# Kernel tuning notes

Hardware: AMD Instinct MI355X
Metric: run time of the kernel (lower is better)

## Reference

```python
import jax, jax.numpy as jnp
import numpy as np

DIM = 1024
HEADS = 16
DIM_HEAD = 64
SEQ = 2048
BATCH = 2
SCALE = DIM_HEAD ** -0.5
NEG = -jnp.finfo(jnp.float32).max


def setup_inputs() -> dict:
    key = jax.random.key(0)
    k1, k2, k3 = jax.random.split(key, 3)
    x = jax.random.normal(k1, (BATCH, SEQ, DIM), dtype=jnp.float32)
    w_qkv = jax.random.normal(k2, (DIM, 3 * HEADS * DIM_HEAD), dtype=jnp.float32) * 0.02
    w_out = jax.random.normal(k3, (HEADS * DIM_HEAD, DIM), dtype=jnp.float32) * 0.02
    b_out = jnp.zeros((DIM,), dtype=jnp.float32)
    return {"x": x, "w_qkv": w_qkv, "w_out": w_out, "b_out": b_out}


def reference(x, w_qkv, w_out, b_out):
    b, n, _ = x.shape
    qkv = x @ w_qkv  # [b, n, 3*h*d]
    q, k, v = jnp.split(qkv, 3, axis=-1)
    def to_heads(t):
        return t.reshape(b, n, HEADS, DIM_HEAD).transpose(0, 2, 1, 3)  # b h n d
    q, k, v = to_heads(q), to_heads(k), to_heads(v)
    q = q * SCALE
    dots = jnp.einsum('bhid,bhjd->bhij', q, k)  # materialized [b,h,n,n] scores
    causal_mask = jnp.triu(jnp.ones((n, n), dtype=bool), k=1)
    dots = jnp.where(causal_mask, NEG, dots)
    attn = jax.nn.softmax(dots, axis=-1)
    out = jnp.einsum('bhij,bhjd->bhid', attn, v)
    out = out.transpose(0, 2, 1, 3).reshape(b, n, HEADS * DIM_HEAD)
    return out @ w_out + b_out
```

## Files before the change

### kernel.cpp

```cpp
#include <hip/hip_runtime.h>
#include <cstdint>

typedef __attribute__((ext_vector_type(8))) short bfrag_t;
typedef __attribute__((ext_vector_type(4))) float f32x4_t;

#define MFMA16(a,b,c) __builtin_amdgcn_mfma_f32_16x16x32_bf16((a),(b),(c),0,0,0)

__device__ __forceinline__ unsigned short f2bf(float f){
  unsigned u = __float_as_uint(f);
  unsigned r = u + 0x7fffu + ((u >> 16) & 1u);
  return (unsigned short)(r >> 16);
}

__device__ __forceinline__ unsigned pk2bf(float a, float b){
  unsigned r;
  asm("v_cvt_pk_bf16_f32 %0, %1, %2" : "=v"(r) : "v"(a), "v"(b));
  return r;
}

__device__ __forceinline__ void gload16(const unsigned short* g, unsigned short* l){
  __builtin_amdgcn_global_load_lds(
      (const __attribute__((address_space(1))) unsigned int*)(const void*)g,
      (__attribute__((address_space(3))) unsigned int*)(void*)l,
      16, 0, 0);
}

__global__ __launch_bounds__(256) void k_prep(
    const float* __restrict__ x,     unsigned short* __restrict__ xbf,
    const float* __restrict__ wqkv,  unsigned short* __restrict__ wqkvT,
    const float* __restrict__ wout,  unsigned short* __restrict__ woutT)
{
  __shared__ unsigned short tile[32][33];
  const int bid = blockIdx.x;
  const int tid = threadIdx.x;

  if (bid < 2048){
    const int n4 = 4096*1024/4;
    int i = bid*256 + tid;
    #pragma unroll
    for(int it=0; it<2; it++, i += 2048*256){
      if (i < n4){
        float4 v = ((const float4*)x)[i];
        ushort4 o;
        o.x = f2bf(v.x); o.y = f2bf(v.y); o.z = f2bf(v.z); o.w = f2bf(v.w);
        ((ushort4*)xbf)[i] = o;
      }
    }
    return;
  }

  const float* in; unsigned short* out; int R, C, idx;
  if (bid < 5120){ in = wqkv; out = wqkvT; R = 1024; C = 3072; idx = bid - 2048; }
  else           { in = wout; out = woutT; R = 1024; C = 1024; idx = bid - 5120; }
  const int nbc = C >> 5;
  const int bc = (idx % nbc) * 32, br = (idx / nbc) * 32;
  const int tx = tid & 31, ty = tid >> 5;
  #pragma unroll
  for(int i=0;i<32;i+=8){
    tile[ty+i][tx] = f2bf(in[(size_t)(br+ty+i)*C + bc + tx]);
  }
  __syncthreads();
  #pragma unroll
  for(int i=0;i<32;i+=8){
    out[(size_t)(bc+ty+i)*R + br + tx] = tile[tx][ty+i];
  }
}

__global__ __launch_bounds__(256) void k_gemm1(
    const unsigned short* __restrict__ A,
    const unsigned short* __restrict__ Bt,
    unsigned short* __restrict__ Qo, unsigned short* __restrict__ Kimg,
    unsigned short* __restrict__ Vimg)
{
  __shared__ unsigned short ldsA[128*64];
  __shared__ unsigned short ldsB[128*64];

  const int tid = threadIdx.x;
  const int lane = tid & 63;
  const int w = tid >> 6;
  const int wr = w >> 1, wc = w & 1;
  const int col16 = lane & 15, g = lane >> 4;

  const int L = blockIdx.x;
  const int bm = (L / 24) * 128;
  const int bn = (L % 24) * 128;
  const int K = 1024;
  const int SWAP = (bn < 2048) ? 1 : 0;

  f32x4_t acc[4][4];
  #pragma unroll
  for(int i=0;i<4;i++)
    #pragma unroll
    for(int j=0;j<4;j++) acc[i][j] = (f32x4_t)0.0f;

  for(int k0=0; k0<K; k0+=64){
    __syncthreads();
    #pragma unroll
    for(int i=0; i<4; i++){
      int u = i*256 + tid;
      int row = u>>3, s = u&7, gs = s ^ (row&7);
      gload16(A + (size_t)(bm+row)*K + k0 + gs*8, ldsA + (i*256 + w*64)*8);
    }
    #pragma unroll
    for(int i=0; i<4; i++){
      int u = i*256 + tid;
      int row = u>>3, s = u&7, gs = s ^ (row&7);
      gload16(Bt + (size_t)(bn+row)*K + k0 + gs*8, ldsB + (i*256 + w*64)*8);
    }
    __syncthreads();
    #pragma unroll
    for(int kk=0; kk<2; kk++){
      bfrag_t af[4], bfr[4];
      #pragma unroll
      for(int mi=0;mi<4;mi++){
        int row = wr*64 + mi*16 + col16;
        int slot = (kk*4 + g) ^ (row&7);
        af[mi] = *(const bfrag_t*)(ldsA + row*64 + slot*8);
      }
      #pragma unroll
      for(int ni=0;ni<4;ni++){
        int row = wc*64 + ni*16 + col16;
        int slot = (kk*4 + g) ^ (row&7);
        bfr[ni] = *(const bfrag_t*)(ldsB + row*64 + slot*8);
      }
      if (SWAP){
        #pragma unroll
        for(int mi=0;mi<4;mi++)
          #pragma unroll
          for(int ni=0;ni<4;ni++)
            acc[mi][ni] = MFMA16(bfr[ni], af[mi], acc[mi][ni]);
      } else {
        #pragma unroll
        for(int mi=0;mi<4;mi++)
          #pragma unroll
          for(int ni=0;ni<4;ni++)
            acc[mi][ni] = MFMA16(af[mi], bfr[ni], acc[mi][ni]);
      }
    }
  }

  if (bn < 2048){
    const int which = bn >> 10;
    #pragma unroll
    for(int mi=0;mi<4;mi++){
      int s_full = bm + wr*64 + mi*16 + col16;
      int b = s_full >> 11, sq = s_full & 2047;
      #pragma unroll
      for(int ni=0;ni<4;ni++){
        int n0 = bn + wc*64 + ni*16 + g*4;
        int h = (n0 & 1023) >> 6;
        int d0 = n0 & 63;
        size_t bh = (size_t)(b*16 + h);
        float v0 = acc[mi][ni][0], v1 = acc[mi][ni][1];
        float v2 = acc[mi][ni][2], v3 = acc[mi][ni][3];
        if (which == 0){
          const float sc = 0.18033688f;
          uint2 pkd; pkd.x = pk2bf(v0*sc, v1*sc); pkd.y = pk2bf(v2*sc, v3*sc);
          *(uint2*)(Qo + (bh*2048 + sq)*64 + d0) = pkd;
        } else {
          int kt = sq >> 6, rr = sq & 63;
          int ks = rr >> 4, c16i = rr & 15;
          int dk = d0 >> 5, g3 = (d0 >> 3) & 3, e0 = d0 & 7;
          uint2 pkd; pkd.x = pk2bf(v0, v1); pkd.y = pk2bf(v2, v3);
          size_t off = bh*131072 + (size_t)kt*4096
                     + (size_t)(ks*2 + dk)*512 + (size_t)(g3*16 + c16i)*8 + e0;
          *(uint2*)(Kimg + off) = pkd;
        }
      }
    }
  } else {
    #pragma unroll
    for(int mi=0;mi<4;mi++){
      int s0 = bm + wr*64 + mi*16 + g*4;
      int b = s0 >> 11, sq0 = s0 & 2047;
      int kt = sq0 >> 6, sc0 = sq0 & 63;
      int jk = sc0 >> 5, g3 = (sc0 >> 3) & 3, e0 = sc0 & 7;
      #pragma unroll
      for(int ni=0;ni<4;ni++){
        int ncol = bn + wc*64 + ni*16 + col16;
        int h = (ncol & 1023) >> 6;
        int d64 = ncol & 63;
        int nimg = d64 >> 4, c16i = d64 & 15;
        size_t bh = (size_t)(b*16 + h);
        uint2 pkd;
        pkd.x = pk2bf(acc[mi][ni][0], acc[mi][ni][1]);
        pkd.y = pk2bf(acc[mi][ni][2], acc[mi][ni][3]);
        size_t off = bh*131072 + (size_t)kt*4096
                   + (size_t)(nimg*2 + jk)*512 + (size_t)(g3*16 + c16i)*8 + e0;
        *(uint2*)(Vimg + off) = pkd;
      }
    }
  }
}

__global__ __launch_bounds__(256) void k_gemm2(
    const unsigned short* __restrict__ A,
    const unsigned short* __restrict__ Bt,
    float* __restrict__ Co, const float* __restrict__ bias)
{
  __shared__ unsigned short ldsA[64*64];
  __shared__ unsigned short ldsB[128*64];

  const int tid = threadIdx.x;
  const int lane = tid & 63;
  const int w = tid >> 6;
  const int wc = w;
  const int col16 = lane & 15, g = lane >> 4;

  const int L = blockIdx.x;
  const int swz = (L & 7) * 64 + (L >> 3);
  const int bm = (swz >> 3) * 64;
  const int bn = (swz & 7) * 128;
  const int K = 1024, N = 1024;

  f32x4_t acc[4][2];
  #pragma unroll
  for(int i=0;i<4;i++)
    #pragma unroll
    for(int j=0;j<2;j++) acc[i][j] = (f32x4_t)0.0f;

  for(int k0=0; k0<K; k0+=64){
    __syncthreads();
    #pragma unroll
    for(int i=0; i<2; i++){
      int u = i*256 + tid;
      int row = u>>3, s = u&7, gs = s ^ (row&7);
      gload16(A + (size_t)(bm+row)*K + k0 + gs*8, ldsA + (i*256 + w*64)*8);
    }
    #pragma unroll
    for(int i=0; i<4; i++){
      int u = i*256 + tid;
      int row = u>>3, s = u&7, gs = s ^ (row&7);
      gload16(Bt + (size_t)(bn+row)*K + k0 + gs*8, ldsB + (i*256 + w*64)*8);
    }
    __syncthreads();
    #pragma unroll
    for(int kk=0; kk<2; kk++){
      bfrag_t af[4], bfr[2];
      #pragma unroll
      for(int mi=0;mi<4;mi++){
        int row = mi*16 + col16;
        int slot = (kk*4 + g) ^ (row&7);
        af[mi] = *(const bfrag_t*)(ldsA + row*64 + slot*8);
      }
      #pragma unroll
      for(int ni=0;ni<2;ni++){
        int row = wc*32 + ni*16 + col16;
        int slot = (kk*4 + g) ^ (row&7);
        bfr[ni] = *(const bfrag_t*)(ldsB + row*64 + slot*8);
      }
      #pragma unroll
      for(int mi=0;mi<4;mi++)
        #pragma unroll
        for(int ni=0;ni<2;ni++)
          acc[mi][ni] = MFMA16(af[mi], bfr[ni], acc[mi][ni]);
    }
  }

  #pragma unroll
  for(int mi=0;mi<4;mi++){
    int mrow = bm + mi*16 + g*4;
    #pragma unroll
    for(int ni=0;ni<2;ni++){
      int ncol = bn + wc*32 + ni*16 + col16;
      float bb = bias[ncol];
      #pragma unroll
      for(int r=0;r<4;r++){
        Co[(size_t)(mrow+r)*N + ncol] = acc[mi][ni][r] + bb;
      }
    }
  }
}

__global__ __launch_bounds__(256, 4) void k_attn(
    const unsigned short* __restrict__ Q,
    const unsigned short* __restrict__ Kimg,
    const unsigned short* __restrict__ Vimg,
    unsigned short* __restrict__ O)
{
  __shared__ unsigned short kls[2*4096];
  __shared__ unsigned short vls[2*4096];
  __shared__ unsigned short plds[4*1024];
  const int lane = threadIdx.x & 63;
  const int w = threadIdx.x >> 6;
  const int col16 = lane & 15, g = lane >> 4;
  const int bh = blockIdx.x;
  const int y = blockIdx.y;
  const int idx = (y & 7)*4 + (y >> 3);
  const int qt = (idx & 1) ? (31 - (idx >> 1)) : (idx >> 1);
  const int b = bh >> 4, h = bh & 15;

  const unsigned short* Qb = Q    + (size_t)bh*2048*64;
  const unsigned short* Kb = Kimg + (size_t)bh*131072;
  const unsigned short* Vb = Vimg + (size_t)bh*131072;
  char* pw = (char*)(plds + w*1024);

  auto stage = [&](int kt, int bsel){
    const unsigned short* gk = Kb + (size_t)kt*4096;
    const unsigned short* gv = Vb + (size_t)kt*4096;
    unsigned short* lk = kls + bsel*4096;
    unsigned short* lv = vls + bsel*4096;
    #pragma unroll
    for(int c=0;c<2;c++){
      int chunk = w*2 + c;
      int u = chunk*64 + lane;
      gload16(gk + u*8, lk + chunk*512);
      gload16(gv + u*8, lv + chunk*512);
    }
  };

  const int qrow0 = qt*64 + w*16;
  const int nkt = qt + 1;
  const int qi = qrow0 + col16;

  bfrag_t qf[2];
  #pragma unroll
  for(int dk=0;dk<2;dk++)
    qf[dk] = *(const bfrag_t*)(Qb + (size_t)(qrow0 + col16)*64 + dk*32 + g*8);

  f32x4_t oaccT[4];
  #pragma unroll
  for(int n=0;n<4;n++) oaccT[n] = (f32x4_t)0.0f;
  float mrun = -1e30f, lrun = 0.f;

  stage(0, 0);
  __syncthreads();

  #pragma unroll 1
  for(int kt=0; kt<nkt; kt++){
    const int cur = kt & 1;
    if (kt+1 < nkt) stage(kt+1, cur^1);

    const bfrag_t* kb = (const bfrag_t*)(kls + cur*4096);
    const bfrag_t* vb = (const bfrag_t*)(vls + cur*4096);

    f32x4_t sacc[4];
    __builtin_amdgcn_s_setprio(1);
    #pragma unroll
    for(int ks=0; ks<4; ks++){
      bfrag_t kf0 = kb[(ks*2+0)*64 + lane];
      bfrag_t kf1 = kb[(ks*2+1)*64 + lane];
      f32x4_t c = (f32x4_t)0.0f;
      c = MFMA16(kf0, qf[0], c);
      c = MFMA16(kf1, qf[1], c);
      sacc[ks] = c;
    }
    __builtin_amdgcn_s_setprio(0);
    if (kt == qt){
      const int kbase = kt*64;
      #pragma unroll
      for(int ks=0; ks<4; ks++)
        #pragma unroll
        for(int r=0;r<4;r++){
          int kj = kbase + ks*16 + g*4 + r;
          if (kj > qi) sacc[ks][r] = -1e30f;
        }
    }
    float pm = fmaxf(
        fmaxf(fmaxf(fmaxf(sacc[0][0],sacc[0][1]),fmaxf(sacc[0][2],sacc[0][3])),
              fmaxf(fmaxf(sacc[1][0],sacc[1][1]),fmaxf(sacc[1][2],sacc[1][3]))),
        fmaxf(fmaxf(fmaxf(sacc[2][0],sacc[2][1]),fmaxf(sacc[2][2],sacc[2][3])),
              fmaxf(fmaxf(sacc[3][0],sacc[3][1]),fmaxf(sacc[3][2],sacc[3][3]))));
    pm = fmaxf(pm, __shfl_xor(pm, 16));
    pm = fmaxf(pm, __shfl_xor(pm, 32));
    if (!__all(pm - mrun <= 11.5415603f)){
      float mnew = fmaxf(mrun, pm);
      float alpha = __builtin_amdgcn_exp2f(mrun - mnew);
      mrun = mnew;
      lrun *= alpha;
      #pragma unroll
      for(int n=0;n<4;n++)
        #pragma unroll
        for(int r=0;r<4;r++)
          oaccT[n][r] *= alpha;
    }
    float rs = 0.f;
    #pragma unroll
    for(int ks=0; ks<4; ks++){
      float p0 = __builtin_amdgcn_exp2f(sacc[ks][0] - mrun);
      float p1 = __builtin_amdgcn_exp2f(sacc[ks][1] - mrun);
      float p2 = __builtin_amdgcn_exp2f(sacc[ks][2] - mrun);
      float p3 = __builtin_amdgcn_exp2f(sacc[ks][3] - mrun);
      rs += (p0+p1)+(p2+p3);
      unsigned w0 = pk2bf(p0, p1);
      unsigned w1 = pk2bf(p2, p3);
      int byte0 = (col16*128 + (ks*16 + g*4)*2) ^ ((col16&7)<<4);
      unsigned long long wd = ((unsigned long long)w1 << 32) | w0;
      *(unsigned long long*)(pw + byte0) = wd;
    }
    rs += __shfl_xor(rs, 16);
    rs += __shfl_xor(rs, 32);
    lrun += rs;
    bfrag_t pf[2];
    #pragma unroll
    for(int jk=0;jk<2;jk++){
      int byteo = (col16*128 + jk*64 + g*16) ^ ((col16&7)<<4);
      pf[jk] = *(const bfrag_t*)(pw + byteo);
    }
    __builtin_amdgcn_s_setprio(1);
    #pragma unroll
    for(int n=0;n<4;n++){
      bfrag_t v0 = vb[(n*2+0)*64 + lane];
      bfrag_t v1 = vb[(n*2+1)*64 + lane];
      oaccT[n] = MFMA16(v0, pf[0], oaccT[n]);
      oaccT[n] = MFMA16(v1, pf[1], oaccT[n]);
    }
    __builtin_amdgcn_s_setprio(0);
    __syncthreads();
  }

  {
    float inv = 1.0f / lrun;
    size_t obase = ((size_t)(b*2048 + qi))*1024 + (size_t)h*64;
    #pragma unroll
    for(int n=0;n<4;n++){
      uint2 pkd;
      pkd.x = pk2bf(oaccT[n][0]*inv, oaccT[n][1]*inv);
      pkd.y = pk2bf(oaccT[n][2]*inv, oaccT[n][3]*inv);
      *(uint2*)(O + obase + n*16 + g*4) = pkd;
    }
  }
}

extern "C" void kernel_launch(void* const* d_in, const int* in_sizes, int n_in,
                              void* d_out, int out_size, void* d_ws, size_t ws_size,
                              hipStream_t stream){
  const float* x     = (const float*)d_in[0];
  const float* w_qkv = (const float*)d_in[1];
  const float* w_out = (const float*)d_in[2];
  const float* b_out = (const float*)d_in[3];
  float* out = (float*)d_out;

  unsigned char* ws = (unsigned char*)d_ws;
  unsigned short* xbf   = (unsigned short*)(ws);
  unsigned short* wqkvT = (unsigned short*)(ws + (size_t)8*1024*1024);
  unsigned short* woutT = (unsigned short*)(ws + (size_t)14*1024*1024);
  unsigned short* Qb    = (unsigned short*)(ws + (size_t)16*1024*1024);
  unsigned short* Kb    = (unsigned short*)(ws + (size_t)24*1024*1024);
  unsigned short* Vtb   = (unsigned short*)(ws + (size_t)32*1024*1024);
  unsigned short* attno = xbf;

  k_prep<<<6144, 256, 0, stream>>>(x, xbf, w_qkv, wqkvT, w_out, woutT);
  k_gemm1<<<768, 256, 0, stream>>>(xbf, wqkvT, Qb, Kb, Vtb);
  k_attn<<<dim3(32, 32), 256, 0, stream>>>(Qb, Kb, Vtb, attno);
  k_gemm2<<<512, 256, 0, stream>>>(attno, woutT, out, b_out);
}
```

Baseline: 112.2 us.

## Triple-buffer QKV GEMM K-loop with async LDS loads and vmcnt waits

Replaces the single-buffered 64-wide K loop of the QKV projection GEMM with a three-stage, 32-wide K pipeline. Global-to-LDS loads for step t+2 are issued while step t computes, and a single barrier per step with partial vmcnt waits replaces the two __syncthreads. The swizzle is adapted to 32-element rows, and s_setprio raises wave priority around the MFMA block. This aims to hide global memory latency behind MFMA work, at the cost of more LDS, hand-counted waitcnt correctness, and half the MFMAs per barrier.

```diff
diff --git a/kernel.cpp b/kernel.cpp
--- a/kernel.cpp
+++ b/kernel.cpp
@@ -72,8 +72,12 @@
     unsigned short* __restrict__ Qo, unsigned short* __restrict__ Kimg,
     unsigned short* __restrict__ Vimg)
 {
-  __shared__ unsigned short ldsA[128*64];
-  __shared__ unsigned short ldsB[128*64];
+  __shared__ unsigned short lA0[128*32];
+  __shared__ unsigned short lA1[128*32];
+  __shared__ unsigned short lA2[128*32];
+  __shared__ unsigned short lB0[128*32];
+  __shared__ unsigned short lB1[128*32];
+  __shared__ unsigned short lB2[128*32];
 
   const int tid = threadIdx.x;
   const int lane = tid & 63;
@@ -93,51 +97,67 @@
     #pragma unroll
     for(int j=0;j<4;j++) acc[i][j] = (f32x4_t)0.0f;
 
-  for(int k0=0; k0<K; k0+=64){
-    __syncthreads();
-    #pragma unroll
-    for(int i=0; i<4; i++){
-      int u = i*256 + tid;
-      int row = u>>3, s = u&7, gs = s ^ (row&7);
-      gload16(A + (size_t)(bm+row)*K + k0 + gs*8, ldsA + (i*256 + w*64)*8);
-    }
-    #pragma unroll
-    for(int i=0; i<4; i++){
-      int u = i*256 + tid;
-      int row = u>>3, s = u&7, gs = s ^ (row&7);
-      gload16(Bt + (size_t)(bn+row)*K + k0 + gs*8, ldsB + (i*256 + w*64)*8);
-    }
-    __syncthreads();
-    #pragma unroll
-    for(int kk=0; kk<2; kk++){
-      bfrag_t af[4], bfr[4];
-      #pragma unroll
-      for(int mi=0;mi<4;mi++){
-        int row = wr*64 + mi*16 + col16;
-        int slot = (kk*4 + g) ^ (row&7);
-        af[mi] = *(const bfrag_t*)(ldsA + row*64 + slot*8);
-      }
-      #pragma unroll
-      for(int ni=0;ni<4;ni++){
-        int row = wc*64 + ni*16 + col16;
-        int slot = (kk*4 + g) ^ (row&7);
-        bfr[ni] = *(const bfrag_t*)(ldsB + row*64 + slot*8);
-      }
-      if (SWAP){
-        #pragma unroll
-        for(int mi=0;mi<4;mi++)
-          #pragma unroll
-          for(int ni=0;ni<4;ni++)
-            acc[mi][ni] = MFMA16(bfr[ni], af[mi], acc[mi][ni]);
-      } else {
-        #pragma unroll
-        for(int mi=0;mi<4;mi++)
-          #pragma unroll
-          for(int ni=0;ni<4;ni++)
-            acc[mi][ni] = MFMA16(af[mi], bfr[ni], acc[mi][ni]);
-      }
-    }
-  }
+#define G1STAGE(KN_, LAS_, LBS_)                                             \
+  { _Pragma("unroll")                                                        \
+    for(int i_=0;i_<2;i_++){                                                 \
+      int u_ = i_*256 + tid;                                                 \
+      int row_ = u_>>2, s_ = u_&3, gs_ = s_ ^ ((row_>>1)&3);                 \
+      gload16(A + (size_t)(bm+row_)*K + (KN_) + gs_*8,                       \
+              (LAS_) + (i_*256 + w*64)*8);                                   \
+    }                                                                        \
+    _Pragma("unroll")                                                        \
+    for(int i_=0;i_<2;i_++){                                                 \
+      int u_ = i_*256 + tid;                                                 \
+      int row_ = u_>>2, s_ = u_&3, gs_ = s_ ^ ((row_>>1)&3);                 \
+      gload16(Bt + (size_t)(bn+row_)*K + (KN_) + gs_*8,                      \
+              (LBS_) + (i_*256 + w*64)*8);                                   \
+    } }
+
+#define G1STEP(T_, LAC_, LBC_, LAS_, LBS_, WAITS_, DOSTAGE_)                 \
+  {                                                                          \
+    asm volatile(WAITS_ ::: "memory");                                       \
+    asm volatile("s_barrier" ::: "memory");                                  \
+    if (DOSTAGE_){ G1STAGE(((T_)+2)*32, LAS_, LBS_); }                       \
+    bfrag_t af_[4], bf_[4];                                                  \
+    _Pragma("unroll")                                                        \
+    for(int mi_=0;mi_<4;mi_++){                                              \
+      int row_ = wr*64 + mi_*16 + col16;                                     \
+      int slot_ = g ^ ((row_>>1)&3);                                         \
+      af_[mi_] = *(const bfrag_t*)((LAC_) + row_*32 + slot_*8);              \
+    }                                                                        \
+    _Pragma("unroll")                                                        \
+    for(int ni_=0;ni_<4;ni_++){                                              \
+      int row_ = wc*64 + ni_*16 + col16;                                     \
+      int slot_ = g ^ ((row_>>1)&3);                                         \
+      bf_[ni_] = *(const bfrag_t*)((LBC_) + row_*32 + slot_*8);              \
+    }                                                                        \
+    __builtin_amdgcn_s_setprio(1);                                           \
+    if (SWAP){                                                               \
+      _Pragma("unroll") for(int mi_=0;mi_<4;mi_++)                           \
+      _Pragma("unroll") for(int ni_=0;ni_<4;ni_++)                           \
+        acc[mi_][ni_] = MFMA16(bf_[ni_], af_[mi_], acc[mi_][ni_]);           \
+    } else {                                                                 \
+      _Pragma("unroll") for(int mi_=0;mi_<4;mi_++)                           \
+      _Pragma("unroll") for(int ni_=0;ni_<4;ni_++)                           \
+        acc[mi_][ni_] = MFMA16(af_[mi_], bf_[ni_], acc[mi_][ni_]);           \
+    }                                                                        \
+    __builtin_amdgcn_s_setprio(0);                                           \
+  }
+
+  G1STAGE(0,  lA0, lB0);
+  G1STAGE(32, lA1, lB1);
+
+  #pragma unroll 1
+  for(int t3=0; t3<30; t3+=3){
+    G1STEP(t3+0, lA0, lB0, lA2, lB2, "s_waitcnt vmcnt(4)", true);
+    G1STEP(t3+1, lA1, lB1, lA0, lB0, "s_waitcnt vmcnt(4)", true);
+    G1STEP(t3+2, lA2, lB2, lA1, lB1, "s_waitcnt vmcnt(4)", true);
+  }
+  G1STEP(30, lA0, lB0, lA2, lB2, "s_waitcnt vmcnt(4)", false);
+  G1STEP(31, lA1, lB1, lA0, lB0, "s_waitcnt vmcnt(0)", false);
+
+#undef G1STEP
+#undef G1STAGE
 
   if (bn < 2048){
     const int which = bn >> 10;
```

Result: slower. 118.2 us (+5.4%).
